# Kernel optimization log

Hardware: AMD Instinct MI355X
Metric: run time of the kernel (lower is better)

## Reference

```python
import jax, jax.numpy as jnp
import numpy as np

N_SAMPLES = 262144
N_FEATURES = 256
N_CLUSTERS = 256


def setup_inputs() -> dict:
    key = jax.random.key(0)
    kx, kc = jax.random.split(key)
    x = jax.random.normal(kx, (N_SAMPLES, N_FEATURES), dtype=jnp.float32)
    centroids = jax.random.normal(kc, (N_CLUSTERS, N_FEATURES), dtype=jnp.float32)
    return {"x": x, "centroids": centroids}


def reference(x, centroids):
    # Squared Euclidean distance to each centroid, computed via the Gram trick
    # to avoid materializing the (n, k, f) broadcasted intermediate.
    # Original: distance = sqrt(sum((x[:,None,:] - c)^2, axis=2)); q = 1/(1+distance^2)
    # sqrt followed by square is the identity on the non-negative distance,
    # so we use the squared distance directly.
    x_sq = jnp.sum(x * x, axis=1, keepdims=True)          # (n, 1)
    c_sq = jnp.sum(centroids * centroids, axis=1)          # (k,)
    cross = x @ centroids.T                                # (n, k)
    sq_dist = jnp.maximum(x_sq - 2.0 * cross + c_sq, 0.0)  # (n, k)
    # Student-t kernel (alpha = 1) and row-normalization -> soft assignments
    q = 1.0 / (1.0 + sq_dist)
    q = q / jnp.sum(q, axis=1, keepdims=True)
    return q
```

## Files before the change

### kernel.cpp

```cpp
#include <hip/hip_runtime.h>
#include <hip/hip_bf16.h>

#define NF 256
#define NC 256
#define NSAMP 262144
#define BM 64
#define NTHREADS 512
#define LDA 264

typedef __attribute__((ext_vector_type(8))) short short8;
typedef __attribute__((ext_vector_type(4))) float floatx4;

__device__ __forceinline__ unsigned short f2bf(float f) {
    unsigned int u = __builtin_bit_cast(unsigned int, f);
    return (unsigned short)((u + 0x7FFFu + ((u >> 16) & 1u)) >> 16);
}

__global__ __launch_bounds__(64)
void prep_centroids(const float* __restrict__ cent,
                    unsigned short* __restrict__ cbf,
                    float* __restrict__ csq)
{
    const int row  = blockIdx.x;
    const int lane = threadIdx.x;
    const floatx4 v = *(const floatx4*)(cent + (size_t)row * NF + lane * 4);
    ushort4 b;
    b.x = f2bf(v.x); b.y = f2bf(v.y); b.z = f2bf(v.z); b.w = f2bf(v.w);
    *(ushort4*)(cbf + (size_t)row * NF + lane * 4) = b;
    float s = v.x * v.x + v.y * v.y + v.z * v.z + v.w * v.w;
    s += __shfl_xor(s, 1);
    s += __shfl_xor(s, 2);
    s += __shfl_xor(s, 4);
    s += __shfl_xor(s, 8);
    s += __shfl_xor(s, 16);
    s += __shfl_xor(s, 32);
    if (lane == 0) csq[row] = s;
}

__global__ __launch_bounds__(NTHREADS, 4)
void cluster_soft_assign(const float* __restrict__ x,
                         const unsigned short* __restrict__ cbf,
                         const float* __restrict__ csq,
                         float* __restrict__ out)
{
    __shared__ __align__(16) unsigned short As[BM * LDA];
    __shared__ __align__(16) float xsq[BM];
    __shared__ __align__(16) float rowsum[BM];

    const int tid  = threadIdx.x;
    const int wave = tid >> 6;
    const int lane = tid & 63;
    const int quad = lane >> 4;
    const int l16  = lane & 15;
    const int row0 = blockIdx.x * BM;

    const int srow = tid >> 3;
    const int sc   = tid & 7;
    {
        float s = 0.f;
        #pragma unroll
        for (int i = 0; i < 8; ++i) {
            const floatx4 v = *(const floatx4*)(x + (size_t)(row0 + srow) * NF + (sc + 8 * i) * 4);
            s += v.x * v.x + v.y * v.y + v.z * v.z + v.w * v.w;
            ushort4 b;
            b.x = f2bf(v.x); b.y = f2bf(v.y); b.z = f2bf(v.z); b.w = f2bf(v.w);
            *(ushort4*)(As + srow * LDA + (sc + 8 * i) * 4) = b;
        }
        s += __shfl_xor(s, 1);
        s += __shfl_xor(s, 2);
        s += __shfl_xor(s, 4);
        if (sc == 0) xsq[srow] = s;
    }
    if (tid < BM) rowsum[tid] = 0.f;

    short8 bfr[2][8];
    #pragma unroll
    for (int j = 0; j < 2; ++j)
        #pragma unroll
        for (int kk = 0; kk < 8; ++kk)
            bfr[j][kk] = *(const short8*)(cbf + ((wave * 32 + j * 16 + l16) << 8) + kk * 32 + quad * 8);

    __syncthreads();

    floatx4 acc[4][2];
    #pragma unroll
    for (int i = 0; i < 4; ++i) {
        acc[i][0] = (floatx4){0.f, 0.f, 0.f, 0.f};
        acc[i][1] = (floatx4){0.f, 0.f, 0.f, 0.f};
    }
    #pragma unroll
    for (int kk = 0; kk < 8; ++kk) {
        #pragma unroll
        for (int i = 0; i < 4; ++i) {
            const short8 afr = *(const short8*)(As + (i * 16 + l16) * LDA + kk * 32 + quad * 8);
            acc[i][0] = __builtin_amdgcn_mfma_f32_16x16x32_bf16(afr, bfr[0][kk], acc[i][0], 0, 0, 0);
            acc[i][1] = __builtin_amdgcn_mfma_f32_16x16x32_bf16(afr, bfr[1][kk], acc[i][1], 0, 0, 0);
        }
    }

    float csv[2];
    csv[0] = csq[wave * 32 + l16];
    csv[1] = csq[wave * 32 + 16 + l16];

    float rs[4][4];
    #pragma unroll
    for (int i = 0; i < 4; ++i) {
        const floatx4 xv = *(const floatx4*)(xsq + i * 16 + quad * 4);
        #pragma unroll
        for (int reg = 0; reg < 4; ++reg) rs[i][reg] = 0.f;
        #pragma unroll
        for (int j = 0; j < 2; ++j) {
            #pragma unroll
            for (int reg = 0; reg < 4; ++reg) {
                float d = xv[reg] - 2.f * acc[i][j][reg] + csv[j];
                d = fmaxf(d, 0.f);
                const float q = __builtin_amdgcn_rcpf(1.f + d);
                acc[i][j][reg] = q;
                rs[i][reg] += q;
            }
        }
    }
    #pragma unroll
    for (int i = 0; i < 4; ++i) {
        #pragma unroll
        for (int reg = 0; reg < 4; ++reg) {
            float v = rs[i][reg];
            v += __shfl_xor(v, 1);
            v += __shfl_xor(v, 2);
            v += __shfl_xor(v, 4);
            v += __shfl_xor(v, 8);
            if (l16 == 0) atomicAdd(&rowsum[i * 16 + quad * 4 + reg], v);
        }
    }
    __syncthreads();

    #pragma unroll
    for (int i = 0; i < 4; ++i) {
        const floatx4 rv = *(const floatx4*)(rowsum + i * 16 + quad * 4);
        floatx4 inv;
        #pragma unroll
        for (int reg = 0; reg < 4; ++reg) inv[reg] = __builtin_amdgcn_rcpf(rv[reg]);
        float* orow = out + (size_t)(row0 + i * 16 + quad * 4) * NC + wave * 32 + l16;
        #pragma unroll
        for (int j = 0; j < 2; ++j)
            #pragma unroll
            for (int reg = 0; reg < 4; ++reg)
                orow[(size_t)reg * NC + j * 16] = acc[i][j][reg] * inv[reg];
    }
}

extern "C" void kernel_launch(void* const* d_in, const int* in_sizes, int n_in,
                              void* d_out, int out_size, void* d_ws, size_t ws_size,
                              hipStream_t stream) {
    const float* x    = (const float*)d_in[0];
    const float* cent = (const float*)d_in[1];
    float* out        = (float*)d_out;

    unsigned short* cbf = (unsigned short*)d_ws;
    float* csq          = (float*)((char*)d_ws + (size_t)NC * NF * 2);

    prep_centroids<<<dim3(NC), dim3(64), 0, stream>>>(cent, cbf, csq);
    cluster_soft_assign<<<dim3(NSAMP / BM), dim3(NTHREADS), 0, stream>>>(x, cbf, csq, out);
}
```

Before: 454.1 us.

## Persistent double-buffered tiles with prefetch and folded -2 centroid scaling

Each block now handles 8 row tiles with 1024 threads (16 waves, each owning 16 centroid columns) and keeps its centroid fragments in registers across all tiles. The next tile's x rows are loaded into registers while the current tile runs its MFMAs, then converted into a second LDS buffer. The -2 factor is folded into the bf16 centroids, which removes a multiply from the epilogue. This amortises centroid loads and block launch cost and hides global load latency. In exchange it cuts the grid to 512 blocks, adds more barriers per tile, and does more shuffle and atomic reductions per wave.

```diff
diff --git a/kernel.cpp b/kernel.cpp
--- a/kernel.cpp
+++ b/kernel.cpp
@@ -1,11 +1,12 @@
 #include <hip/hip_runtime.h>
-#include <hip/hip_bf16.h>
 
 #define NF 256
 #define NC 256
 #define NSAMP 262144
 #define BM 64
-#define NTHREADS 512
+#define TILES 8
+#define NBLK 512
+#define NTHREADS 1024
 #define LDA 264
 
 typedef __attribute__((ext_vector_type(8))) short short8;
@@ -14,6 +15,12 @@
 __device__ __forceinline__ unsigned short f2bf(float f) {
     unsigned int u = __builtin_bit_cast(unsigned int, f);
     return (unsigned short)((u + 0x7FFFu + ((u >> 16) & 1u)) >> 16);
+}
+
+__device__ __forceinline__ void lds_sync() {
+    asm volatile("s_waitcnt lgkmcnt(0)" ::: "memory");
+    __builtin_amdgcn_sched_barrier(0);
+    __builtin_amdgcn_s_barrier();
 }
 
 __global__ __launch_bounds__(64)
@@ -25,7 +32,8 @@
     const int lane = threadIdx.x;
     const floatx4 v = *(const floatx4*)(cent + (size_t)row * NF + lane * 4);
     ushort4 b;
-    b.x = f2bf(v.x); b.y = f2bf(v.y); b.z = f2bf(v.z); b.w = f2bf(v.w);
+    b.x = f2bf(-2.f * v.x); b.y = f2bf(-2.f * v.y);
+    b.z = f2bf(-2.f * v.z); b.w = f2bf(-2.f * v.w);
     *(ushort4*)(cbf + (size_t)row * NF + lane * 4) = b;
     float s = v.x * v.x + v.y * v.y + v.z * v.z + v.w * v.w;
     s += __shfl_xor(s, 1);
@@ -43,109 +51,122 @@
                          const float* __restrict__ csq,
                          float* __restrict__ out)
 {
-    __shared__ __align__(16) unsigned short As[BM * LDA];
-    __shared__ __align__(16) float xsq[BM];
-    __shared__ __align__(16) float rowsum[BM];
+    __shared__ __align__(16) unsigned short As[2][BM * LDA];
+    __shared__ __align__(16) float xsq[2][BM];
+    __shared__ __align__(16) float rowsum[2][BM];
 
     const int tid  = threadIdx.x;
     const int wave = tid >> 6;
     const int lane = tid & 63;
     const int quad = lane >> 4;
     const int l16  = lane & 15;
-    const int row0 = blockIdx.x * BM;
+    const int srow = tid >> 4;
+    const int sc   = tid & 15;
+    const int col0 = wave << 4;
 
-    const int srow = tid >> 3;
-    const int sc   = tid & 7;
+    const size_t brow = (size_t)blockIdx.x * (BM * TILES);
+
+    short8 bfr[8];
+    #pragma unroll
+    for (int kk = 0; kk < 8; ++kk)
+        bfr[kk] = *(const short8*)(cbf + ((col0 + l16) << 8) + kk * 32 + quad * 8);
+    const float csv = csq[col0 + l16];
+
+    if (tid < 2 * BM) ((float*)rowsum)[tid] = 0.f;
+
+    floatx4 L[4];
     {
+        const float* xr = x + (brow + srow) * NF + sc * 4;
+        #pragma unroll
+        for (int i = 0; i < 4; ++i) L[i] = *(const floatx4*)(xr + i * 64);
         float s = 0.f;
         #pragma unroll
-        for (int i = 0; i < 8; ++i) {
-            const floatx4 v = *(const floatx4*)(x + (size_t)(row0 + srow) * NF + (sc + 8 * i) * 4);
+        for (int i = 0; i < 4; ++i) {
+            const floatx4 v = L[i];
             s += v.x * v.x + v.y * v.y + v.z * v.z + v.w * v.w;
             ushort4 b;
             b.x = f2bf(v.x); b.y = f2bf(v.y); b.z = f2bf(v.z); b.w = f2bf(v.w);
-            *(ushort4*)(As + srow * LDA + (sc + 8 * i) * 4) = b;
+            *(ushort4*)(&As[0][srow * LDA + (sc + 16 * i) * 4]) = b;
         }
         s += __shfl_xor(s, 1);
         s += __shfl_xor(s, 2);
         s += __shfl_xor(s, 4);
-        if (sc == 0) xsq[srow] = s;
+        s += __shfl_xor(s, 8);
+        if (sc == 0) xsq[0][srow] = s;
     }
-    if (tid < BM) rowsum[tid] = 0.f;
+    lds_sync();
 
-    short8 bfr[2][8];
-    #pragma unroll
-    for (int j = 0; j < 2; ++j)
+    int cur = 0;
+    for (int t = 0; t < TILES; ++t) {
+        if (t + 1 < TILES) {
+            const float* xr = x + (brow + (size_t)(t + 1) * BM + srow) * NF + sc * 4;
+            #pragma unroll
+            for (int i = 0; i < 4; ++i) L[i] = *(const floatx4*)(xr + i * 64);
+            __builtin_amdgcn_sched_barrier(0);
+        }
+        if (tid < BM) rowsum[cur ^ 1][tid] = 0.f;
+
+        floatx4 acc[4];
         #pragma unroll
-        for (int kk = 0; kk < 8; ++kk)
-            bfr[j][kk] = *(const short8*)(cbf + ((wave * 32 + j * 16 + l16) << 8) + kk * 32 + quad * 8);
+        for (int i = 0; i < 4; ++i) acc[i] = (floatx4){0.f, 0.f, 0.f, 0.f};
+        const unsigned short* as = As[cur];
+        #pragma unroll
+        for (int kk = 0; kk < 8; ++kk) {
+            #pragma unroll
+            for (int i = 0; i < 4; ++i) {
+                const short8 afr = *(const short8*)(as + (i * 16 + l16) * LDA + kk * 32 + quad * 8);
+                acc[i] = __builtin_amdgcn_mfma_f32_16x16x32_bf16(afr, bfr[kk], acc[i], 0, 0, 0);
+            }
+        }
 
-    __syncthreads();
-
-    floatx4 acc[4][2];
-    #pragma unroll
-    for (int i = 0; i < 4; ++i) {
-        acc[i][0] = (floatx4){0.f, 0.f, 0.f, 0.f};
-        acc[i][1] = (floatx4){0.f, 0.f, 0.f, 0.f};
-    }
-    #pragma unroll
-    for (int kk = 0; kk < 8; ++kk) {
         #pragma unroll
         for (int i = 0; i < 4; ++i) {
-            const short8 afr = *(const short8*)(As + (i * 16 + l16) * LDA + kk * 32 + quad * 8);
-            acc[i][0] = __builtin_amdgcn_mfma_f32_16x16x32_bf16(afr, bfr[0][kk], acc[i][0], 0, 0, 0);
-            acc[i][1] = __builtin_amdgcn_mfma_f32_16x16x32_bf16(afr, bfr[1][kk], acc[i][1], 0, 0, 0);
-        }
-    }
-
-    float csv[2];
-    csv[0] = csq[wave * 32 + l16];
-    csv[1] = csq[wave * 32 + 16 + l16];
-
-    float rs[4][4];
-    #pragma unroll
-    for (int i = 0; i < 4; ++i) {
-        const floatx4 xv = *(const floatx4*)(xsq + i * 16 + quad * 4);
-        #pragma unroll
-        for (int reg = 0; reg < 4; ++reg) rs[i][reg] = 0.f;
-        #pragma unroll
-        for (int j = 0; j < 2; ++j) {
+            const floatx4 xv = *(const floatx4*)(&xsq[cur][i * 16 + quad * 4]);
             #pragma unroll
             for (int reg = 0; reg < 4; ++reg) {
-                float d = xv[reg] - 2.f * acc[i][j][reg] + csv[j];
-                d = fmaxf(d, 0.f);
+                float d = fmaxf(xv[reg] + acc[i][reg] + csv, 0.f);
                 const float q = __builtin_amdgcn_rcpf(1.f + d);
-                acc[i][j][reg] = q;
-                rs[i][reg] += q;
+                acc[i][reg] = q;
+                float v = q;
+                v += __shfl_xor(v, 1);
+                v += __shfl_xor(v, 2);
+                v += __shfl_xor(v, 4);
+                v += __shfl_xor(v, 8);
+                if (l16 == 0) atomicAdd(&rowsum[cur][i * 16 + quad * 4 + reg], v);
             }
         }
-    }
-    #pragma unroll
-    for (int i = 0; i < 4; ++i) {
-        #pragma unroll
-        for (int reg = 0; reg < 4; ++reg) {
-            float v = rs[i][reg];
-            v += __shfl_xor(v, 1);
-            v += __shfl_xor(v, 2);
-            v += __shfl_xor(v, 4);
-            v += __shfl_xor(v, 8);
-            if (l16 == 0) atomicAdd(&rowsum[i * 16 + quad * 4 + reg], v);
+        lds_sync();
+
+        {
+            const size_t rt = brow + (size_t)t * BM;
+            #pragma unroll
+            for (int i = 0; i < 4; ++i) {
+                const floatx4 rv = *(const floatx4*)(&rowsum[cur][i * 16 + quad * 4]);
+                float* orow = out + (rt + i * 16 + quad * 4) * NC + col0 + l16;
+                #pragma unroll
+                for (int reg = 0; reg < 4; ++reg)
+                    orow[(size_t)reg * NC] = acc[i][reg] * __builtin_amdgcn_rcpf(rv[reg]);
+            }
         }
-    }
-    __syncthreads();
 
-    #pragma unroll
-    for (int i = 0; i < 4; ++i) {
-        const floatx4 rv = *(const floatx4*)(rowsum + i * 16 + quad * 4);
-        floatx4 inv;
-        #pragma unroll
-        for (int reg = 0; reg < 4; ++reg) inv[reg] = __builtin_amdgcn_rcpf(rv[reg]);
-        float* orow = out + (size_t)(row0 + i * 16 + quad * 4) * NC + wave * 32 + l16;
-        #pragma unroll
-        for (int j = 0; j < 2; ++j)
+        if (t + 1 < TILES) {
+            float s = 0.f;
             #pragma unroll
-            for (int reg = 0; reg < 4; ++reg)
-                orow[(size_t)reg * NC + j * 16] = acc[i][j][reg] * inv[reg];
+            for (int i = 0; i < 4; ++i) {
+                const floatx4 v = L[i];
+                s += v.x * v.x + v.y * v.y + v.z * v.z + v.w * v.w;
+                ushort4 b;
+                b.x = f2bf(v.x); b.y = f2bf(v.y); b.z = f2bf(v.z); b.w = f2bf(v.w);
+                *(ushort4*)(&As[cur ^ 1][srow * LDA + (sc + 16 * i) * 4]) = b;
+            }
+            s += __shfl_xor(s, 1);
+            s += __shfl_xor(s, 2);
+            s += __shfl_xor(s, 4);
+            s += __shfl_xor(s, 8);
+            if (sc == 0) xsq[cur ^ 1][srow] = s;
+            lds_sync();
+            cur ^= 1;
+        }
     }
 }
 
@@ -160,5 +181,5 @@
     float* csq          = (float*)((char*)d_ws + (size_t)NC * NF * 2);
 
     prep_centroids<<<dim3(NC), dim3(64), 0, stream>>>(cent, cbf, csq);
-    cluster_soft_assign<<<dim3(NSAMP / BM), dim3(NTHREADS), 0, stream>>>(x, cbf, csq, out);
+    cluster_soft_assign<<<dim3(NBLK), dim3(NTHREADS), 0, stream>>>(x, cbf, csq, out);
 }
```

Result: no change. 458.5 us (+1.0%).
